# Kernel optimization log

Measured on AMD Instinct MI355X. Metric: run time of the kernel, lower is better.

The kernel has to match this reference:

```python
import jax, jax.numpy as jnp
import numpy as np

B, T, D_IN, D_HID, D_OUT, N_CAT = 128, 64, 1024, 1024, 1536, 32


def setup_inputs() -> dict:
    key = jax.random.key(0)
    kx, kw1, kw2, kc = jax.random.split(key, 4)
    x = jax.random.normal(kx, (B, T, D_IN), dtype=jnp.float32)
    W1 = 0.02 * jax.random.normal(kw1, (N_CAT, D_IN, D_HID), dtype=jnp.float32)
    b1 = jnp.zeros((N_CAT, D_HID), dtype=jnp.float32)
    W2 = 0.02 * jax.random.normal(kw2, (N_CAT, D_HID, D_OUT), dtype=jnp.float32)
    b2 = jnp.zeros((N_CAT, D_OUT), dtype=jnp.float32)
    cat_ids = jax.random.randint(kc, (B,), 0, N_CAT)
    return {"x": x, "W1": W1, "b1": b1, "W2": W2, "b2": b2, "cat_ids": cat_ids}


def reference(x, W1, b1, W2, b2, cat_ids):
    # CategorySpecificLinear: gather per-sample expert weights, then batched matmul.
    # Layer 1: (B,T,D_in) @ (B,D_in,D_hid) + (B,1,D_hid)
    h = jnp.einsum('btd,bdh->bth', x, W1[cat_ids]) + b1[cat_ids][:, None, :]
    h = jax.nn.relu(h)
    # Layer 2: (B,T,D_hid) @ (B,D_hid,D_out) + (B,1,D_out)
    out = jnp.einsum('bth,bho->bto', h, W2[cat_ids]) + b2[cat_ids][:, None, :]
    return out
```

## Files before the change

### kernel.cpp

```cpp
#include <hip/hip_runtime.h>
#include <stdint.h>

#define NB    128
#define TT    64
#define KTOT  1024
#define DHID  1024
#define DOUT  1536
#define NCAT  32

#define BK    64
#define TN    128
#define PADR  72
#define NGMAX 64

typedef unsigned short u16;
typedef __attribute__((ext_vector_type(8))) short bf16x8;
typedef __attribute__((ext_vector_type(4))) float f32x4;
typedef __attribute__((ext_vector_type(4))) unsigned int uint4v;
typedef __attribute__((ext_vector_type(4))) float float4v;

__device__ __forceinline__ float bf2f(u16 u) {
    unsigned int x = ((unsigned int)u) << 16;
    return __builtin_bit_cast(float, x);
}
__device__ __forceinline__ unsigned int f2bf_u32(float f) {
    unsigned int x = __builtin_bit_cast(unsigned int, f);
    return (x + 0x7FFFu + ((x >> 16) & 1u)) >> 16;
}
__device__ __forceinline__ u16 f2bf(float f) { return (u16)f2bf_u32(f); }

__device__ int g_is_f32;

__global__ void detect_dtype(const unsigned int* __restrict__ xw) {
    const int lane = threadIdx.x;
    const unsigned int w = xw[lane * 64];
    const unsigned int e = (w >> 7) & 0xFF;
    const unsigned long long m = __ballot(e >= 120 && e <= 132);
    if (lane == 0) g_is_f32 = (__popcll(m) < 32) ? 1 : 0;
}

__device__ __forceinline__ void gload16(const void* g, void* l) {
    __builtin_amdgcn_global_load_lds(
        (const __attribute__((address_space(1))) void*)g,
        (__attribute__((address_space(3))) void*)l, 16, 0, 0);
}

__global__ void prep_all(const void* __restrict__ x, u16* __restrict__ xb,
                         const int* __restrict__ cid,
                         int* __restrict__ gcat, int* __restrict__ gbat) {
    __shared__ int sh_f32;
    const int t = threadIdx.x;
    if (t < 64) {
        const unsigned int w = ((const unsigned int*)x)[t * 64];
        const unsigned int e = (w >> 7) & 0xFF;
        const unsigned long long m = __ballot(e >= 120 && e <= 132);
        if (t == 0) sh_f32 = (__popcll(m) < 32) ? 1 : 0;
    }
    __syncthreads();
    const bool f32 = (sh_f32 != 0);
    if (blockIdx.x == 0 && t == 0) g_is_f32 = f32 ? 1 : 0;

    const size_t base = ((size_t)blockIdx.x * 256 + t) * 8;
    if (f32) {
        const float* s = (const float*)x + base;
        float4v f0 = *(const float4v*)s;
        float4v f1 = *(const float4v*)(s + 4);
        uint4v v;
        v.x = f2bf_u32(f0.x) | (f2bf_u32(f0.y) << 16);
        v.y = f2bf_u32(f0.z) | (f2bf_u32(f0.w) << 16);
        v.z = f2bf_u32(f1.x) | (f2bf_u32(f1.y) << 16);
        v.w = f2bf_u32(f1.z) | (f2bf_u32(f1.w) << 16);
        *(uint4v*)&xb[base] = v;
    } else {
        *(uint4v*)&xb[base] = *(const uint4v*)((const u16*)x + base);
    }

    if (blockIdx.x == 0) {
        __shared__ int cl[NB];
        __shared__ int cnt[NCAT], start[NCAT], gbase[NCAT];
        __shared__ int sorted[NB];
        if (t < NB) cl[t] = cid[t];
        if (t < NGMAX) gcat[t] = -1;
        gbat[t] = -1;
        __syncthreads();
        if (t < NCAT) {
            int c = 0;
            for (int i = 0; i < NB; ++i) c += (cl[i] == t) ? 1 : 0;
            cnt[t] = c;
        }
        __syncthreads();
        if (t == 0) {
            int s = 0, g = 0;
            for (int c = 0; c < NCAT; ++c) {
                start[c] = s; s += cnt[c];
                gbase[c] = g; g += (cnt[c] + 3) >> 2;
            }
        }
        __syncthreads();
        if (t < NB) {
            const int myc = cl[t];
            int r = 0;
            for (int i = 0; i < t; ++i) r += (cl[i] == myc) ? 1 : 0;
            sorted[start[myc] + r] = t;
        }
        __syncthreads();
        if (t < NCAT) {
            const int n = cnt[t], ng = (n + 3) >> 2;
            for (int j = 0; j < ng; ++j) {
                const int g = gbase[t] + j;
                gcat[g] = t;
                for (int k = 0; k < 4; ++k) {
                    const int idx = j * 4 + k;
                    gbat[g * 4 + k] = (idx < n) ? sorted[start[t] + idx] : -1;
                }
            }
        }
    }
}

template<int NW, bool RELU, bool OUT_DYN>
__global__ __launch_bounds__(512, 4)
void gemm_grp(const u16* __restrict__ A,
              const void* __restrict__ Win,
              const void* __restrict__ BiasIn,
              void* __restrict__ Cout,
              const int* __restrict__ gcat,
              const int* __restrict__ gbat)
{
    constexpr int NT   = NW / TN;
    constexpr int NTIL = KTOT / 32;
    __shared__ __align__(16) u16 As[2][4 * TT * 32];
    __shared__ __align__(16) u16 Bs[2][TN * 32];

    const int bid = blockIdx.x;
    const int qq  = bid >> 3;
    const int nt  = qq % NT;
    const int g   = (bid & 7) + 8 * (qq / NT);
    const int cat = gcat[g];
    if (cat < 0) return;

    const bool f32 = (g_is_f32 != 0);
    const int t    = threadIdx.x;
    const int wave = t >> 6;
    const int lane = t & 63;
    const int l16  = lane & 15;
    const int q    = lane >> 4;
    const int wm   = wave & 1;
    const int wn   = wave >> 1;

    int  bl[4]; bool lv[4];
#pragma unroll
    for (int k2 = 0; k2 < 4; ++k2) { int v = gbat[g * 4 + k2]; lv[k2] = (v >= 0); bl[k2] = v; }
#pragma unroll
    for (int k2 = 1; k2 < 4; ++k2) if (!lv[k2]) bl[k2] = bl[0];

    const int tt   = t & 255;
    const int arow = tt >> 2;
    const int asc  = (((tt & 3) ^ ((tt >> 2) & 3) ^ ((tt >> 4) & 3)) << 3);
    const int sA0  = wave >> 2, sA1 = 2 + (wave >> 2);
    const u16* aG0 = A + (size_t)bl[sA0] * (TT * KTOT) + (size_t)arow * KTOT + asc;
    const u16* aG1 = A + (size_t)bl[sA1] * (TT * KTOT) + (size_t)arow * KTOT + asc;

    const int bn  = t & 127;
    const int kc  = t >> 7;
    const int wch = ((kc ^ (bn & 3) ^ ((bn >> 2) & 3)) << 4);
    const size_t wOff = (size_t)cat * ((size_t)KTOT * NW) + (size_t)(kc * 8) * NW
                        + (size_t)nt * TN + bn;
    const float* w32 = (const float*)Win + wOff;
    const u16*   w16 = (const u16*)Win + wOff;

    const int CH = ((q ^ (l16 & 3) ^ ((l16 >> 2) & 3)) << 4);

    f32x4 acc[4][2][2];
#pragma unroll
    for (int bt = 0; bt < 4; ++bt)
#pragma unroll
        for (int im = 0; im < 2; ++im)
#pragma unroll
            for (int in = 0; in < 2; ++in)
                acc[bt][im][in] = (f32x4){0.f, 0.f, 0.f, 0.f};

    unsigned int wr[8];

    auto W_ISSUE = [&](int kk) {
        if (f32) {
            const float* ws = w32 + (size_t)kk * NW;
#pragma unroll
            for (int j = 0; j < 8; ++j)
                wr[j] = __builtin_bit_cast(unsigned int, ws[(size_t)j * NW]);
        } else {
            const u16* ws = w16 + (size_t)kk * NW;
#pragma unroll
            for (int j = 0; j < 8; ++j) wr[j] = ws[(size_t)j * NW];
        }
    };
    auto W_PACK = [&](int pb) {
        unsigned int p[4];
#pragma unroll
        for (int i = 0; i < 4; ++i) {
            unsigned int lo, hi;
            if (f32) {
                lo = f2bf_u32(__builtin_bit_cast(float, wr[2*i]));
                hi = f2bf_u32(__builtin_bit_cast(float, wr[2*i+1]));
            } else { lo = wr[2*i]; hi = wr[2*i+1]; }
            p[i] = lo | (hi << 16);
        }
        uint4v v; v.x = p[0]; v.y = p[1]; v.z = p[2]; v.w = p[3];
        *(uint4v*)((char*)&Bs[pb][0] + bn * 64 + wch) = v;
    };
    auto A_ISSUE = [&](int pb, int kk) {
        char* ab = (char*)&As[pb][0] + wave * 1024;
        gload16(aG0 + kk, ab);
        gload16(aG1 + kk, ab + 8192);
    };
    auto COMPUTE = [&](int pb) {
        const char* bsb = (const char*)&Bs[pb][0];
        const int nrow = wn * 32 + l16;
        bf16x8 bb0 = *(const bf16x8*)(bsb + nrow * 64 + CH);
        bf16x8 bb1 = *(const bf16x8*)(bsb + (nrow + 16) * 64 + CH);
        const char* asb = (const char*)&As[pb][0] + (wm * 32 + l16) * 64 + CH;
#pragma unroll
        for (int bt = 0; bt < 4; ++bt) {
            bf16x8 a0 = *(const bf16x8*)(asb + bt * 4096);
            bf16x8 a1 = *(const bf16x8*)(asb + bt * 4096 + 1024);
            acc[bt][0][0] = __builtin_amdgcn_mfma_f32_16x16x32_bf16(a0, bb0, acc[bt][0][0], 0, 0, 0);
            acc[bt][0][1] = __builtin_amdgcn_mfma_f32_16x16x32_bf16(a0, bb1, acc[bt][0][1], 0, 0, 0);
            acc[bt][1][0] = __builtin_amdgcn_mfma_f32_16x16x32_bf16(a1, bb0, acc[bt][1][0], 0, 0, 0);
            acc[bt][1][1] = __builtin_amdgcn_mfma_f32_16x16x32_bf16(a1, bb1, acc[bt][1][1], 0, 0, 0);
        }
    };

    W_ISSUE(0);
    A_ISSUE(0, 0);
    asm volatile("s_waitcnt vmcnt(2)" ::: "memory");
    W_PACK(0);

#pragma unroll 2
    for (int tl = 0; tl < NTIL; ++tl) {
        const int cur = tl & 1;
        if (tl + 1 < NTIL) {
            W_ISSUE((tl + 1) * 32);
            A_ISSUE(cur ^ 1, (tl + 1) * 32);
            asm volatile("s_waitcnt vmcnt(10) lgkmcnt(0)" ::: "memory");
        } else {
            asm volatile("s_waitcnt vmcnt(0) lgkmcnt(0)" ::: "memory");
        }
        __builtin_amdgcn_s_barrier();
        __builtin_amdgcn_s_setprio(1);
        COMPUTE(cur);
        __builtin_amdgcn_s_setprio(0);
        if (tl + 1 < NTIL) {
            asm volatile("s_waitcnt vmcnt(2)" ::: "memory");
            W_PACK(cur ^ 1);
            __builtin_amdgcn_s_barrier();
        }
    }

    const float* bias32 = (const float*)BiasIn + (size_t)cat * NW + (size_t)nt * TN;
    const u16*   bias16 = (const u16*)BiasIn + (size_t)cat * NW + (size_t)nt * TN;
#pragma unroll
    for (int in = 0; in < 2; ++in) {
        const int ncol = wn * 32 + in * 16 + l16;
        const float bv = f32 ? bias32[ncol] : bf2f(bias16[ncol]);
#pragma unroll
        for (int bt = 0; bt < 4; ++bt) {
            if (!lv[bt]) continue;
            const size_t cOff = (size_t)bl[bt] * (TT * NW) + (size_t)nt * TN + ncol;
#pragma unroll
            for (int im = 0; im < 2; ++im) {
#pragma unroll
                for (int r = 0; r < 4; ++r) {
                    const int m = wm * 32 + im * 16 + q * 4 + r;
                    float v = acc[bt][im][in][r] + bv;
                    if (RELU) v = fmaxf(v, 0.f);
                    if (OUT_DYN && f32) ((float*)Cout)[cOff + (size_t)m * NW] = v;
                    else                ((u16*)Cout)[cOff + (size_t)m * NW] = f2bf(v);
                }
            }
        }
    }
}

template<int NW, bool RELU, bool A_DYN, bool OUT_DYN>
__global__ __launch_bounds__(256, 4)
void gemm_cat(const void* __restrict__ Ain,
              const void* __restrict__ Win,
              const void* __restrict__ BiasIn,
              void* __restrict__ Cout,
              const int* __restrict__ cat_ids)
{
    constexpr int NT = NW / TN;
    __shared__ u16 As[TT * PADR];
    __shared__ u16 Bs[TN * PADR];

    const bool f32  = (g_is_f32 != 0);
    const bool aF32 = A_DYN && f32;
    const bool oF32 = OUT_DYN && f32;

    const int b   = blockIdx.x / NT;
    const int nt  = blockIdx.x % NT;
    const int cat = cat_ids[b];

    const int tid  = threadIdx.x;
    const int lane = tid & 63;
    const int l16  = lane & 15;
    const int q    = lane >> 4;
    const int wave = tid >> 6;
    const int wm   = wave & 1;
    const int wn   = wave >> 1;

    const size_t aOff = (size_t)b * (TT * KTOT);
    const u16*   Ab16 = (const u16*)Ain + aOff;
    const float* Ab32 = (const float*)Ain + aOff;
    const size_t wOff = (size_t)cat * ((size_t)KTOT * NW) + (size_t)nt * TN;
    const u16*   Wb16 = (const u16*)Win + wOff;
    const float* Wb32 = (const float*)Win + wOff;

    const int ar = tid >> 2;
    const int ac = (tid & 3) * 16;
    const int bn  = tid & 127;
    const int bk0 = tid >> 7;

    f32x4 acc[2][4];
#pragma unroll
    for (int im = 0; im < 2; ++im)
#pragma unroll
        for (int in = 0; in < 4; ++in)
            acc[im][in] = (f32x4){0.f, 0.f, 0.f, 0.f};

    for (int kk = 0; kk < KTOT; kk += BK) {
        if (!aF32) {
            const u16* src = Ab16 + ar * KTOT + kk + ac;
            uint4v v0 = *(const uint4v*)(src);
            uint4v v1 = *(const uint4v*)(src + 8);
            *(uint4v*)&As[ar * PADR + ac]     = v0;
            *(uint4v*)&As[ar * PADR + ac + 8] = v1;
        } else {
            const float* src = Ab32 + ar * KTOT + kk + ac;
            float4v f0 = *(const float4v*)(src);
            float4v f1 = *(const float4v*)(src + 4);
            float4v f2 = *(const float4v*)(src + 8);
            float4v f3 = *(const float4v*)(src + 12);
            uint4v v0, v1;
            v0.x = f2bf_u32(f0.x) | (f2bf_u32(f0.y) << 16);
            v0.y = f2bf_u32(f0.z) | (f2bf_u32(f0.w) << 16);
            v0.z = f2bf_u32(f1.x) | (f2bf_u32(f1.y) << 16);
            v0.w = f2bf_u32(f1.z) | (f2bf_u32(f1.w) << 16);
            v1.x = f2bf_u32(f2.x) | (f2bf_u32(f2.y) << 16);
            v1.y = f2bf_u32(f2.z) | (f2bf_u32(f2.w) << 16);
            v1.z = f2bf_u32(f3.x) | (f2bf_u32(f3.y) << 16);
            v1.w = f2bf_u32(f3.z) | (f2bf_u32(f3.w) << 16);
            *(uint4v*)&As[ar * PADR + ac]     = v0;
            *(uint4v*)&As[ar * PADR + ac + 8] = v1;
        }
#pragma unroll
        for (int i = 0; i < 4; ++i) {
            const int kc = bk0 + i * 2;
            unsigned int s[8];
            if (!f32) {
                const u16* src = Wb16 + (size_t)(kk + kc * 8) * NW + bn;
#pragma unroll
                for (int j = 0; j < 8; ++j) s[j] = src[(size_t)j * NW];
            } else {
                const float* src = Wb32 + (size_t)(kk + kc * 8) * NW + bn;
#pragma unroll
                for (int j = 0; j < 8; ++j) s[j] = f2bf_u32(src[(size_t)j * NW]);
            }
            uint4v v;
            v.x = s[0] | (s[1] << 16);
            v.y = s[2] | (s[3] << 16);
            v.z = s[4] | (s[5] << 16);
            v.w = s[6] | (s[7] << 16);
            *(uint4v*)&Bs[bn * PADR + kc * 8] = v;
        }
        __syncthreads();

#pragma unroll
        for (int s = 0; s < 2; ++s) {
            bf16x8 a[2], bb[4];
#pragma unroll
            for (int im = 0; im < 2; ++im)
                a[im] = *(const bf16x8*)&As[(wm * 32 + im * 16 + l16) * PADR + s * 32 + q * 8];
#pragma unroll
            for (int in = 0; in < 4; ++in)
                bb[in] = *(const bf16x8*)&Bs[(wn * 64 + in * 16 + l16) * PADR + s * 32 + q * 8];
#pragma unroll
            for (int im = 0; im < 2; ++im)
#pragma unroll
                for (int in = 0; in < 4; ++in)
                    acc[im][in] = __builtin_amdgcn_mfma_f32_16x16x32_bf16(
                        a[im], bb[in], acc[im][in], 0, 0, 0);
        }
        __syncthreads();
    }

    const u16*   bias16 = (const u16*)BiasIn + (size_t)cat * NW + nt * TN;
    const float* bias32 = (const float*)BiasIn + (size_t)cat * NW + nt * TN;
    const size_t cOff = (size_t)b * TT * NW + (size_t)nt * TN;
    u16*   C16 = (u16*)Cout + cOff;
    float* C32 = (float*)Cout + cOff;
#pragma unroll
    for (int in = 0; in < 4; ++in) {
        const int ncol = wn * 64 + in * 16 + l16;
        const float bv = f32 ? bias32[ncol] : bf2f(bias16[ncol]);
#pragma unroll
        for (int im = 0; im < 2; ++im) {
#pragma unroll
            for (int r = 0; r < 4; ++r) {
                const int m = wm * 32 + im * 16 + q * 4 + r;
                float v = acc[im][in][r] + bv;
                if (RELU) v = fmaxf(v, 0.f);
                if (oF32) C32[(size_t)m * NW + ncol] = v;
                else      C16[(size_t)m * NW + ncol] = f2bf(v);
            }
        }
    }
}

extern "C" void kernel_launch(void* const* d_in, const int* in_sizes, int n_in,
                              void* d_out, int out_size, void* d_ws, size_t ws_size,
                              hipStream_t stream) {
    const void* x   = d_in[0];
    const void* W1  = d_in[1];
    const void* b1  = d_in[2];
    const void* W2  = d_in[3];
    const void* b2  = d_in[4];
    const int*  cid = (const int*)d_in[5];

    const size_t XB_BYTES = (size_t)NB * TT * KTOT * 2;
    const size_t NEED = 2 * XB_BYTES + 4096;

    if (ws_size >= NEED) {
        u16* xb   = (u16*)d_ws;
        u16* h    = (u16*)((char*)d_ws + XB_BYTES);
        int* gcat = (int*)((char*)d_ws + 2 * XB_BYTES);
        int* gbat = gcat + NGMAX;

        prep_all<<<4096, 256, 0, stream>>>(x, xb, cid, gcat, gbat);
        gemm_grp<DHID, true,  false><<<NGMAX * (DHID / TN), 512, 0, stream>>>(
            xb, W1, b1, (void*)h, gcat, gbat);
        gemm_grp<DOUT, false, true ><<<NGMAX * (DOUT / TN), 512, 0, stream>>>(
            h, W2, b2, d_out, gcat, gbat);
    } else {
        u16* h = (u16*)d_ws;
        detect_dtype<<<1, 64, 0, stream>>>((const unsigned int*)x);
        gemm_cat<DHID, true,  true,  false><<<NB * (DHID / TN), 256, 0, stream>>>(
            x, W1, b1, (void*)h, cid);
        gemm_cat<DOUT, false, false, true ><<<NB * (DOUT / TN), 256, 0, stream>>>(
            (const void*)h, W2, b2, d_out, cid);
    }
}
```

Measured before the change: 509.0 us.

## Deepen grouped GEMM pipeline to prefetch two K-tiles ahead with triple-buffered A

The K loop now prefetches weights and activations two tiles ahead, using a third shared-memory A buffer and two alternating weight register sets. One barrier per iteration is removed because packing into the other B buffer no longer needs a separate sync. The block-to-tile mapping is also changed so the eight consecutive block IDs spread across groups instead of sharing one group. The deeper pipeline aims to hide global load latency, at the cost of extra LDS and registers, which may reduce occupancy. The reduced synchronisation also risks a race on the double-buffered Bs.

```diff
diff --git a/kernel.cpp b/kernel.cpp
--- a/kernel.cpp
+++ b/kernel.cpp
@@ -129,13 +129,14 @@
 {
     constexpr int NT   = NW / TN;
     constexpr int NTIL = KTOT / 32;
-    __shared__ __align__(16) u16 As[2][4 * TT * 32];
+    __shared__ __align__(16) u16 As[3][4 * TT * 32];
     __shared__ __align__(16) u16 Bs[2][TN * 32];
 
-    const int bid = blockIdx.x;
-    const int qq  = bid >> 3;
-    const int nt  = qq % NT;
-    const int g   = (bid & 7) + 8 * (qq / NT);
+    const int nwg = NGMAX * NT;
+    int bid = blockIdx.x;
+    bid = (bid & 7) * (nwg >> 3) + (bid >> 3);
+    const int g   = bid / NT;
+    const int nt  = bid % NT;
     const int cat = gcat[g];
     if (cat < 0) return;
 
@@ -180,9 +181,9 @@
             for (int in = 0; in < 2; ++in)
                 acc[bt][im][in] = (f32x4){0.f, 0.f, 0.f, 0.f};
 
-    unsigned int wr[8];
-
-    auto W_ISSUE = [&](int kk) {
+    unsigned int wrE[8], wrO[8];
+
+    auto W_ISSUE = [&](int kk, unsigned int (&wr)[8]) {
         if (f32) {
             const float* ws = w32 + (size_t)kk * NW;
 #pragma unroll
@@ -194,7 +195,7 @@
             for (int j = 0; j < 8; ++j) wr[j] = ws[(size_t)j * NW];
         }
     };
-    auto W_PACK = [&](int pb) {
+    auto W_PACK = [&](unsigned int (&wr)[8], int pb) {
         unsigned int p[4];
 #pragma unroll
         for (int i = 0; i < 4; ++i) {
@@ -213,12 +214,12 @@
         gload16(aG0 + kk, ab);
         gload16(aG1 + kk, ab + 8192);
     };
-    auto COMPUTE = [&](int pb) {
+    auto COMPUTE = [&](int pa, int pb) {
         const char* bsb = (const char*)&Bs[pb][0];
         const int nrow = wn * 32 + l16;
         bf16x8 bb0 = *(const bf16x8*)(bsb + nrow * 64 + CH);
         bf16x8 bb1 = *(const bf16x8*)(bsb + (nrow + 16) * 64 + CH);
-        const char* asb = (const char*)&As[pb][0] + (wm * 32 + l16) * 64 + CH;
+        const char* asb = (const char*)&As[pa][0] + (wm * 32 + l16) * 64 + CH;
 #pragma unroll
         for (int bt = 0; bt < 4; ++bt) {
             bf16x8 a0 = *(const bf16x8*)(asb + bt * 4096);
@@ -230,30 +231,32 @@
         }
     };
 
-    W_ISSUE(0);
-    A_ISSUE(0, 0);
-    asm volatile("s_waitcnt vmcnt(2)" ::: "memory");
-    W_PACK(0);
-
-#pragma unroll 2
-    for (int tl = 0; tl < NTIL; ++tl) {
-        const int cur = tl & 1;
-        if (tl + 1 < NTIL) {
-            W_ISSUE((tl + 1) * 32);
-            A_ISSUE(cur ^ 1, (tl + 1) * 32);
-            asm volatile("s_waitcnt vmcnt(10) lgkmcnt(0)" ::: "memory");
-        } else {
-            asm volatile("s_waitcnt vmcnt(0) lgkmcnt(0)" ::: "memory");
-        }
+    auto STEP = [&](int tl, unsigned int (&wrI)[8], unsigned int (&wrP)[8]) {
+        if (tl == NTIL - 1) asm volatile("s_waitcnt vmcnt(0) lgkmcnt(0)" ::: "memory");
+        else                asm volatile("s_waitcnt vmcnt(10) lgkmcnt(0)" ::: "memory");
         __builtin_amdgcn_s_barrier();
+        if (tl + 2 < NTIL) {
+            W_ISSUE((tl + 2) * 32, wrI);
+            A_ISSUE((tl + 2) % 3, (tl + 2) * 32);
+        }
         __builtin_amdgcn_s_setprio(1);
-        COMPUTE(cur);
+        COMPUTE(tl % 3, tl & 1);
         __builtin_amdgcn_s_setprio(0);
         if (tl + 1 < NTIL) {
-            asm volatile("s_waitcnt vmcnt(2)" ::: "memory");
-            W_PACK(cur ^ 1);
-            __builtin_amdgcn_s_barrier();
-        }
+            if (tl + 2 < NTIL) asm volatile("s_waitcnt vmcnt(12)" ::: "memory");
+            else               asm volatile("s_waitcnt vmcnt(2)" ::: "memory");
+            W_PACK(wrP, (tl + 1) & 1);
+        }
+    };
+
+    W_ISSUE(0, wrE);  A_ISSUE(0, 0);
+    W_ISSUE(32, wrO); A_ISSUE(1, 32);
+    asm volatile("s_waitcnt vmcnt(12)" ::: "memory");
+    W_PACK(wrE, 0);
+
+    for (int tl = 0; tl < NTIL; tl += 2) {
+        STEP(tl,     wrE, wrO);
+        STEP(tl + 1, wrO, wrE);
     }
 
     const float* bias32 = (const float*)BiasIn + (size_t)cat * NW + (size_t)nt * TN;
```

Result: no change. 499.6 us (-1.9%).

## Shrink grouped GEMM N-tile to 64 with 256 threads and skip empty batch slots

Applied to the files above, without the earlier changes.

Halves the grouped GEMM output tile width from 128 to 64 columns and the block size from 512 to 256 threads, which doubles the grid. Each wave now loads the A rows for one batch slot, and both the loads and the MFMAs are skipped for unused slots in a group. Block indices are remapped so that consecutive workgroups are spread across groups. The hand-tuned s_waitcnt/s_barrier pipeline and setprio are replaced by plain __syncthreads, which may lose load/compute overlap and reloads the A tile twice as often per output column.

```diff
diff --git a/kernel.cpp b/kernel.cpp
--- a/kernel.cpp
+++ b/kernel.cpp
@@ -10,6 +10,7 @@
 
 #define BK    64
 #define TN    128
+#define TNG   64
 #define PADR  72
 #define NGMAX 64
 
@@ -119,7 +120,7 @@
 }
 
 template<int NW, bool RELU, bool OUT_DYN>
-__global__ __launch_bounds__(512, 4)
+__global__ __launch_bounds__(256, 4)
 void gemm_grp(const u16* __restrict__ A,
               const void* __restrict__ Win,
               const void* __restrict__ BiasIn,
@@ -127,15 +128,16 @@
               const int* __restrict__ gcat,
               const int* __restrict__ gbat)
 {
-    constexpr int NT   = NW / TN;
+    constexpr int NT   = NW / TNG;
     constexpr int NTIL = KTOT / 32;
     __shared__ __align__(16) u16 As[2][4 * TT * 32];
-    __shared__ __align__(16) u16 Bs[2][TN * 32];
-
-    const int bid = blockIdx.x;
-    const int qq  = bid >> 3;
-    const int nt  = qq % NT;
-    const int g   = (bid & 7) + 8 * (qq / NT);
+    __shared__ __align__(16) u16 Bs[2][TNG * 32];
+
+    const int nwg = NGMAX * NT;
+    int bid = blockIdx.x;
+    bid = (bid & 7) * (nwg >> 3) + (bid >> 3);
+    const int g   = bid / NT;
+    const int nt  = bid % NT;
     const int cat = gcat[g];
     if (cat < 0) return;
 
@@ -154,18 +156,15 @@
 #pragma unroll
     for (int k2 = 1; k2 < 4; ++k2) if (!lv[k2]) bl[k2] = bl[0];
 
-    const int tt   = t & 255;
-    const int arow = tt >> 2;
-    const int asc  = (((tt & 3) ^ ((tt >> 2) & 3) ^ ((tt >> 4) & 3)) << 3);
-    const int sA0  = wave >> 2, sA1 = 2 + (wave >> 2);
-    const u16* aG0 = A + (size_t)bl[sA0] * (TT * KTOT) + (size_t)arow * KTOT + asc;
-    const u16* aG1 = A + (size_t)bl[sA1] * (TT * KTOT) + (size_t)arow * KTOT + asc;
-
-    const int bn  = t & 127;
-    const int kc  = t >> 7;
+    const int csrc = (lane & 3) ^ ((lane >> 2) & 3) ^ ((lane >> 4) & 3);
+    const u16* aG = A + (size_t)bl[wave] * (TT * KTOT)
+                      + (size_t)(lane >> 2) * KTOT + csrc * 8;
+
+    const int bn  = t & 63;
+    const int kc  = t >> 6;
     const int wch = ((kc ^ (bn & 3) ^ ((bn >> 2) & 3)) << 4);
     const size_t wOff = (size_t)cat * ((size_t)KTOT * NW) + (size_t)(kc * 8) * NW
-                        + (size_t)nt * TN + bn;
+                        + (size_t)nt * TNG + bn;
     const float* w32 = (const float*)Win + wOff;
     const u16*   w16 = (const u16*)Win + wOff;
 
@@ -209,9 +208,12 @@
         *(uint4v*)((char*)&Bs[pb][0] + bn * 64 + wch) = v;
     };
     auto A_ISSUE = [&](int pb, int kk) {
-        char* ab = (char*)&As[pb][0] + wave * 1024;
-        gload16(aG0 + kk, ab);
-        gload16(aG1 + kk, ab + 8192);
+        if (lv[wave]) {
+            char* ab = (char*)&As[pb][0] + wave * 4096;
+#pragma unroll
+            for (int j = 0; j < 4; ++j)
+                gload16(aG + (size_t)j * (16 * KTOT) + kk, ab + j * 1024);
+        }
     };
     auto COMPUTE = [&](int pb) {
         const char* bsb = (const char*)&Bs[pb][0];
@@ -221,6 +223,7 @@
         const char* asb = (const char*)&As[pb][0] + (wm * 32 + l16) * 64 + CH;
 #pragma unroll
         for (int bt = 0; bt < 4; ++bt) {
+            if (!lv[bt]) continue;
             bf16x8 a0 = *(const bf16x8*)(asb + bt * 4096);
             bf16x8 a1 = *(const bf16x8*)(asb + bt * 4096 + 1024);
             acc[bt][0][0] = __builtin_amdgcn_mfma_f32_16x16x32_bf16(a0, bb0, acc[bt][0][0], 0, 0, 0);
@@ -232,8 +235,8 @@
 
     W_ISSUE(0);
     A_ISSUE(0, 0);
-    asm volatile("s_waitcnt vmcnt(2)" ::: "memory");
     W_PACK(0);
+    __syncthreads();
 
 #pragma unroll 2
     for (int tl = 0; tl < NTIL; ++tl) {
@@ -241,23 +244,14 @@
         if (tl + 1 < NTIL) {
             W_ISSUE((tl + 1) * 32);
             A_ISSUE(cur ^ 1, (tl + 1) * 32);
-            asm volatile("s_waitcnt vmcnt(10) lgkmcnt(0)" ::: "memory");
-        } else {
-            asm volatile("s_waitcnt vmcnt(0) lgkmcnt(0)" ::: "memory");
-        }
-        __builtin_amdgcn_s_barrier();
-        __builtin_amdgcn_s_setprio(1);
+        }
         COMPUTE(cur);
-        __builtin_amdgcn_s_setprio(0);
-        if (tl + 1 < NTIL) {
-            asm volatile("s_waitcnt vmcnt(2)" ::: "memory");
-            W_PACK(cur ^ 1);
-            __builtin_amdgcn_s_barrier();
-        }
-    }
-
-    const float* bias32 = (const float*)BiasIn + (size_t)cat * NW + (size_t)nt * TN;
-    const u16*   bias16 = (const u16*)BiasIn + (size_t)cat * NW + (size_t)nt * TN;
+        if (tl + 1 < NTIL) W_PACK(cur ^ 1);
+        __syncthreads();
+    }
+
+    const float* bias32 = (const float*)BiasIn + (size_t)cat * NW + (size_t)nt * TNG;
+    const u16*   bias16 = (const u16*)BiasIn + (size_t)cat * NW + (size_t)nt * TNG;
 #pragma unroll
     for (int in = 0; in < 2; ++in) {
         const int ncol = wn * 32 + in * 16 + l16;
@@ -265,7 +259,7 @@
 #pragma unroll
         for (int bt = 0; bt < 4; ++bt) {
             if (!lv[bt]) continue;
-            const size_t cOff = (size_t)bl[bt] * (TT * NW) + (size_t)nt * TN + ncol;
+            const size_t cOff = (size_t)bl[bt] * (TT * NW) + (size_t)nt * TNG + ncol;
 #pragma unroll
             for (int im = 0; im < 2; ++im) {
 #pragma unroll
@@ -437,9 +431,9 @@
         int* gbat = gcat + NGMAX;
 
         prep_all<<<4096, 256, 0, stream>>>(x, xb, cid, gcat, gbat);
-        gemm_grp<DHID, true,  false><<<NGMAX * (DHID / TN), 512, 0, stream>>>(
+        gemm_grp<DHID, true,  false><<<NGMAX * (DHID / TNG), 256, 0, stream>>>(
             xb, W1, b1, (void*)h, gcat, gbat);
-        gemm_grp<DOUT, false, true ><<<NGMAX * (DOUT / TN), 512, 0, stream>>>(
+        gemm_grp<DOUT, false, true ><<<NGMAX * (DOUT / TNG), 256, 0, stream>>>(
             h, W2, b2, d_out, gcat, gbat);
     } else {
         u16* h = (u16*)d_ws;
```

Result: slower. 520.4 us (+2.2%).
